# Optimization experiments

Measured on AMD Instinct MI355X. Metric: run time of the kernel, lower is better.

Reference implementation:

```python
import jax, jax.numpy as jnp
import numpy as np

N, C, H, W = 4, 256, 32, 32
NH = 2                      # att_nhead
HD = C // NH                # 128 per-head dim
MAX_DIS = 7
WS = 2 * MAX_DIS + 1        # 15 window side
WW = WS * WS                # 225 window positions
T = (C / NH) ** 0.5


def _gather_idx(h, w):
    # idx[wpos, m]: flat index into zero-padded (h+14, w+14) grid of the
    # neighbor at window offset wpos for query pixel m (== F.unfold semantics)
    pw = w + 2 * MAX_DIS
    dy, dx = np.meshgrid(np.arange(WS), np.arange(WS), indexing='ij')
    ys, xs = np.meshgrid(np.arange(h), np.arange(w), indexing='ij')
    idx = (dy.reshape(-1, 1) + ys.reshape(1, -1)) * pw + (dx.reshape(-1, 1) + xs.reshape(1, -1))
    return jnp.asarray(idx, dtype=jnp.int32)  # [WW, h*w]


def setup_inputs() -> dict:
    key = jax.random.key(0)
    ks = jax.random.split(key, 14)
    s = 0.02
    return {
        'q': jax.random.normal(ks[0], (N, C, H, W), jnp.float32),
        'k': jax.random.normal(ks[1], (N, C, H, W), jnp.float32),
        'v': jax.random.normal(ks[2], (N, C, H, W), jnp.float32),
        'Wq': jax.random.normal(ks[3], (C, C), jnp.float32) * s,
        'bq': jnp.zeros((C,), jnp.float32),
        'Wk': jax.random.normal(ks[4], (C, C), jnp.float32) * s,
        'bk': jnp.zeros((C,), jnp.float32),
        'Wv': jax.random.normal(ks[5], (C, C), jnp.float32) * s,
        'bv': jnp.zeros((C,), jnp.float32),
        'Wrel': jax.random.normal(ks[6], (NH, WW, HD), jnp.float32) * s,   # grouped 1x1 conv
        'brel': jnp.zeros((NH * WW,), jnp.float32),
        'V_bias': jax.random.normal(ks[7], (NH, HD, WW), jnp.float32) * s,
        'Wfc': jax.random.normal(ks[8], (C, C), jnp.float32) * s,
        'bfc': jnp.zeros((C,), jnp.float32),
    }


def _conv1x1(x, Wt, b):
    return jnp.einsum('nchw,dc->ndhw', x, Wt) + b[None, :, None, None]


def reference(q, k, v, Wq, bq, Wk, bk, Wv, bv, Wrel, brel, V_bias, Wfc, bfc):
    n, c, h, w = q.shape
    hw = h * w
    idx = _gather_idx(h, w)                                   # [WW, hw]
    pad = ((0, 0), (0, 0), (0, 0), (MAX_DIS, MAX_DIS), (MAX_DIS, MAX_DIS))

    q = _conv1x1(q, Wq, bq)
    k = _conv1x1(k, Wk, bk)
    v = _conv1x1(v, Wv, bv)

    # grouped 1x1 conv: relative position logits, [n, NH, WW, hw]
    rel = jnp.einsum('ngcxy,gwc->ngwxy', q.reshape(n, NH, HD, h, w), Wrel)
    rel = rel + brel.reshape(NH, WW)[None, :, :, None, None]
    rel = rel.reshape(n, NH, WW, hw)

    qs = (q / T).reshape(n, NH, HD, hw)

    # unfold K via zero-pad + gather: [n, NH, HD, WW, hw]
    k_pad = jnp.pad(k.reshape(n, NH, HD, h, w), pad).reshape(n, NH, HD, -1)
    k_un = k_pad[..., idx]
    qk = jnp.einsum('ngcm,ngcwm->ngwm', qs, k_un) + rel

    # boundary mask: neighbor inside the original image
    valid = jnp.pad(jnp.ones((h, w), jnp.float32), MAX_DIS).reshape(-1)[idx] > 0
    qk = jnp.where(valid[None, None], qk, jnp.float32(-1e8))
    attn = jax.nn.softmax(qk, axis=2)                         # over window positions

    agg_bias = jnp.einsum('ngwm,gcw->mngc', attn, V_bias).reshape(hw, n, c)

    # local2global scatter + dense einsum == gather of zero-padded V
    v_pad = jnp.pad(v.reshape(n, NH, HD, h, w), pad).reshape(n, NH, HD, -1)
    v_un = v_pad[..., idx]                                    # [n, NH, HD, WW, hw]
    agg_value = jnp.einsum('ngwm,ngcwm->mngc', attn, v_un).reshape(hw, n, c)

    out = (agg_value + agg_bias) @ Wfc.T + bfc                # [hw, n, c]
    return out
```

## Files before the change

### kernel.cpp

```cpp
#include <hip/hip_runtime.h>
#include <math.h>


typedef __attribute__((ext_vector_type(8))) short short8;
typedef __attribute__((ext_vector_type(4))) short short4v;
typedef __attribute__((ext_vector_type(4))) float floatx4;

__device__ __forceinline__ short f2bf(float f) {
    unsigned u = __float_as_uint(f);
    unsigned r = (u + 0x7fffu + ((u >> 16) & 1u)) >> 16;
    return (short)r;
}
__device__ __forceinline__ float bf2f(short s) {
    return __uint_as_float(((unsigned)(unsigned short)s) << 16);
}

__global__ __launch_bounds__(64)
void conv_w(const float* __restrict__ Wq, const float* __restrict__ Wk,
            const float* __restrict__ Wv, const float* __restrict__ Wfc,
            const float* __restrict__ Wrel, const float* __restrict__ Vb,
            short* __restrict__ Whi, short* __restrict__ Wlo,
            short* __restrict__ Wrh, short* __restrict__ Wrl,
            short* __restrict__ Vbh, short* __restrict__ Vbl)
{
    const int lane = threadIdx.x;
    const int n16 = lane & 15, quad = lane >> 4;
    const int z = blockIdx.z;

    if (z < 4) {
        const float* W = (z == 0 ? Wq : z == 1 ? Wk : z == 2 ? Wv : Wfc);
        const int dt = blockIdx.x, kc = blockIdx.y;
        const int d = dt * 16 + n16, cb = kc * 32 + quad * 8;
        float4 w0 = *(const float4*)&W[d * 256 + cb];
        float4 w1 = *(const float4*)&W[d * 256 + cb + 4];
        float f[8] = {w0.x, w0.y, w0.z, w0.w, w1.x, w1.y, w1.z, w1.w};
        short8 h8, l8;
#pragma unroll
        for (int j = 0; j < 8; ++j) {
            short hb = f2bf(f[j]);
            h8[j] = hb;
            l8[j] = f2bf(f[j] - bf2f(hb));
        }
        long off = (long)z * 65536 + (((long)(dt * 8 + kc) * 64) + lane) * 8;
        *(short8*)(Whi + off) = h8;
        *(short8*)(Wlo + off) = l8;
    } else if (z < 6) {
        const int g = z - 4;
        const int wt = blockIdx.x, kc = blockIdx.y;
        if (wt >= 15 || kc >= 4) return;
        const int w = wt * 16 + n16;
        const int cb = kc * 32 + quad * 8;
        float f[8] = {0.f, 0.f, 0.f, 0.f, 0.f, 0.f, 0.f, 0.f};
        if (w < 225) {
            float4 w0 = *(const float4*)&Wrel[(long)(g * 225 + w) * 128 + cb];
            float4 w1 = *(const float4*)&Wrel[(long)(g * 225 + w) * 128 + cb + 4];
            f[0] = w0.x; f[1] = w0.y; f[2] = w0.z; f[3] = w0.w;
            f[4] = w1.x; f[5] = w1.y; f[6] = w1.z; f[7] = w1.w;
        }
        short8 h8, l8;
#pragma unroll
        for (int j = 0; j < 8; ++j) {
            short hb = f2bf(f[j]);
            h8[j] = hb;
            l8[j] = f2bf(f[j] - bf2f(hb));
        }
        long off = (long)g * 30720 + (((long)(wt * 4 + kc) * 64) + lane) * 8;
        *(short8*)(Wrh + off) = h8;
        *(short8*)(Wrl + off) = l8;
    } else {
        const int g = z - 6;
        const int dt = blockIdx.x, wk = blockIdx.y;
        if (dt >= 8) return;
        const int ch = dt * 16 + n16;
        const int w0 = wk * 32 + quad * 8;
        float f[8];
#pragma unroll
        for (int j = 0; j < 8; ++j) {
            int w = w0 + j;
            f[j] = (w < 225) ? Vb[(long)(g * 128 + ch) * 225 + w] : 0.f;
        }
        short8 h8, l8;
#pragma unroll
        for (int j = 0; j < 8; ++j) {
            short hb = f2bf(f[j]);
            h8[j] = hb;
            l8[j] = f2bf(f[j] - bf2f(hb));
        }
        long off = (((long)(g * 128 + ch)) << 8) + w0;
        *(short8*)(Vbh + off) = h8;
        *(short8*)(Vbl + off) = l8;
    }
}

__global__ __launch_bounds__(256)
void mfma_proj(const float* __restrict__ q, const float* __restrict__ k,
               const float* __restrict__ v,
               const short* __restrict__ Whi, const short* __restrict__ Wlo,
               const float* __restrict__ bq, const float* __restrict__ bk,
               const float* __restrict__ bv,
               short* __restrict__ qhi, short* __restrict__ qlo,
               short* __restrict__ khi, short* __restrict__ klo,
               short* __restrict__ vhi, short* __restrict__ vlo)
{
    __shared__ float st[256 * 17];
    const int tid = threadIdx.x;
    const int wave = tid >> 6, lane = tid & 63;
    const int n16 = lane & 15, quad = lane >> 4;
    const int mt16 = blockIdx.x, z = blockIdx.y;
    const int sel = z >> 2, batch = z & 3;

    const float* X = (sel == 0 ? q : sel == 1 ? k : v) + ((long)batch << 18);

    {
        const float* src = X + ((long)tid << 10) + mt16 * 16;
        float4 a0 = *(const float4*)(src);
        float4 a1 = *(const float4*)(src + 4);
        float4 a2 = *(const float4*)(src + 8);
        float4 a3 = *(const float4*)(src + 12);
        float* d = &st[tid * 17];
        d[0] = a0.x; d[1] = a0.y; d[2] = a0.z; d[3] = a0.w;
        d[4] = a1.x; d[5] = a1.y; d[6] = a1.z; d[7] = a1.w;
        d[8] = a2.x; d[9] = a2.y; d[10] = a2.z; d[11] = a2.w;
        d[12] = a3.x; d[13] = a3.y; d[14] = a3.z; d[15] = a3.w;
    }

    const float* bias = (sel == 0 ? bq : sel == 1 ? bk : bv);
    float bbv[4][4];
#pragma unroll
    for (int i = 0; i < 4; ++i) {
        float4 b4 = *(const float4*)&bias[(wave * 4 + i) * 16 + quad * 4];
        bbv[i][0] = b4.x; bbv[i][1] = b4.y; bbv[i][2] = b4.z; bbv[i][3] = b4.w;
    }
    __syncthreads();

    floatx4 acc[4] = {{0.f,0.f,0.f,0.f},{0.f,0.f,0.f,0.f},
                      {0.f,0.f,0.f,0.f},{0.f,0.f,0.f,0.f}};
    const long abase = (long)sel * 65536 + (long)lane * 8;
#pragma unroll
    for (int kc = 0; kc < 8; ++kc) {
        short8 bh, bl;
        const float* col = &st[(kc * 32 + quad * 8) * 17 + n16];
#pragma unroll
        for (int j = 0; j < 8; ++j) {
            float f = col[j * 17];
            short hb = f2bf(f);
            bh[j] = hb;
            bl[j] = f2bf(f - bf2f(hb));
        }
#pragma unroll
        for (int i = 0; i < 4; ++i) {
            const int dt = wave * 4 + i;
            short8 ahi = *(const short8*)(Whi + abase + (long)(dt * 8 + kc) * 512);
            short8 alo = *(const short8*)(Wlo + abase + (long)(dt * 8 + kc) * 512);
            acc[i] = __builtin_amdgcn_mfma_f32_16x16x32_bf16(ahi, bh, acc[i], 0, 0, 0);
            acc[i] = __builtin_amdgcn_mfma_f32_16x16x32_bf16(ahi, bl, acc[i], 0, 0, 0);
            acc[i] = __builtin_amdgcn_mfma_f32_16x16x32_bf16(alo, bh, acc[i], 0, 0, 0);
        }
    }

    if (sel == 2) {
        const int m = mt16 * 16 + n16;
        const int yq = m >> 5, col = (m & 31) + 8;
#pragma unroll
        for (int i = 0; i < 4; ++i) {
            const int dt = wave * 4 + i;
#pragma unroll
            for (int r = 0; r < 4; ++r) {
                const int ch = dt * 16 + quad * 4 + r;
                const int gg = ch >> 7, chh = ch & 127;
                float f = acc[i][r] + bbv[i][r];
                short hb = f2bf(f);
                short lb = f2bf(f - bf2f(hb));
                long o = (((long)((batch * 2 + gg) * 128 + chh) * 32 + yq)) * 48 + col;
                vhi[o] = hb;
                vlo[o] = lb;
            }
        }
        {
            const int prow = mt16 >> 1, side = mt16 & 1;
            const int gg = tid >> 7, chp = tid & 127;
            long po = (((long)((batch * 2 + gg) * 128 + chp) * 32 + prow)) * 48 + side * 40;
            short8 zz = {0,0,0,0,0,0,0,0};
            *(short8*)(vhi + po) = zz;
            *(short8*)(vlo + po) = zz;
        }
        return;
    }

    __syncthreads();
    float* tile = st;
#pragma unroll
    for (int i = 0; i < 4; ++i) {
        const int dt = wave * 4 + i;
#pragma unroll
        for (int r = 0; r < 4; ++r)
            tile[n16 * 257 + dt * 16 + quad * 4 + r] = acc[i][r] + bbv[i][r];
    }
    __syncthreads();

    const float scale = (sel == 1) ? 0.08838834764831845f : 1.0f;
    const int m_l = tid >> 4, c16 = (tid & 15) * 16;
    const int m = mt16 * 16 + m_l;
    short* oh = sel ? khi : qhi;
    short* ol = sel ? klo : qlo;
#pragma unroll
    for (int half = 0; half < 2; ++half) {
        const int cg = c16 + half * 8;
        short8 h8, l8;
#pragma unroll
        for (int j = 0; j < 8; ++j) {
            float f = tile[m_l * 257 + cg + j] * scale;
            short hb = f2bf(f);
            h8[j] = hb;
            l8[j] = f2bf(f - bf2f(hb));
        }
        const int g = cg >> 7, ch = cg & 127;
        const long base = (((long)(batch * 2 + g) << 10) + m) * 128 + ch;
        *(short8*)(oh + base) = h8;
        *(short8*)(ol + base) = l8;
    }
}

__global__ __launch_bounds__(256)
void scores_pv(const short* __restrict__ qhi, const short* __restrict__ qlo,
               const short* __restrict__ khi, const short* __restrict__ klo,
               const short* __restrict__ Wrh, const short* __restrict__ Wrl,
               const float* __restrict__ brel,
               const short* __restrict__ vhi, const short* __restrict__ vlo,
               const short* __restrict__ Vbh, const short* __restrict__ Vbl,
               short* __restrict__ AGhi, short* __restrict__ AGlo)
{
    __shared__ __align__(16) float qk[16 * 241];
    __shared__ __align__(16) short pah[16 * 264];
    __shared__ __align__(16) short pal[16 * 264];
    __shared__ float invl[16];

    const int tid = threadIdx.x;
    const int wave = tid >> 6, lane = tid & 63;
    const int lin = blockIdx.x;
    const int bz  = lin & 7;
    const int yy  = lin >> 3;
    const int y   = yy >> 1;
    const int xt  = yy & 1;
    const int g = bz & 1;
    const int x0 = xt * 16;

    const int n16 = lane & 15, quad = lane >> 4;
    const long qbase = (((long)bz << 10) + y * 32 + x0 + n16) * 128 + quad * 8;
    short8 a_hi[4], a_lo[4];
#pragma unroll
    for (int ch = 0; ch < 4; ++ch) {
        a_hi[ch] = *(const short8*)(qhi + qbase + ch * 32);
        a_lo[ch] = *(const short8*)(qlo + qbase + ch * 32);
    }

    for (int wt = wave; wt < 15; wt += 4) {
        const short* Ah = Wrh + (long)g * 30720 + ((long)(wt * 4) * 64 + lane) * 8;
        const short* Al = Wrl + (long)g * 30720 + ((long)(wt * 4) * 64 + lane) * 8;
        floatx4 racc = {0.f, 0.f, 0.f, 0.f};
#pragma unroll
        for (int kc = 0; kc < 4; ++kc) {
            short8 whh = *(const short8*)(Ah + kc * 512);
            short8 wll = *(const short8*)(Al + kc * 512);
            racc = __builtin_amdgcn_mfma_f32_16x16x32_bf16(whh, a_hi[kc], racc, 0, 0, 0);
            racc = __builtin_amdgcn_mfma_f32_16x16x32_bf16(whh, a_lo[kc], racc, 0, 0, 0);
            racc = __builtin_amdgcn_mfma_f32_16x16x32_bf16(wll, a_hi[kc], racc, 0, 0, 0);
        }
#pragma unroll
        for (int r = 0; r < 4; ++r) {
            int w = wt * 16 + quad * 4 + r;
            if (w < 225) {
                int dy = w / 15, dx = w - dy * 15;
                qk[n16 * 241 + dy * 16 + dx] = racc[r] + brel[g * 225 + w];
            }
        }
    }
    __syncthreads();

    for (int e = tid; e < 16 * 241; e += 256) {
        int px = e / 241, idx = e - px * 241;
        int dy = idx >> 4, dx = idx & 15;
        int hy = y + dy - 7, hx = x0 + px + dx - 7;
        bool valid = (dx < 15) && (dy < 15) &&
                     (hy >= 0) && (hy < 32) && (hx >= 0) && (hx < 32);
        if (!valid) qk[e] = -1e8f;
    }
    __syncthreads();

    for (int dy = wave; dy < 15; dy += 4) {
        const int ky = y + dy - 7;
        if (ky < 0 || ky > 31) continue;
#pragma unroll
        for (int kxt = 0; kxt < 2; ++kxt) {
            const int kxg = x0 - 8 + kxt * 16 + n16;
            const long kb = (((long)bz << 10) + ky * 32 + kxg) * 128 + quad * 8;
            floatx4 acc = {0.f, 0.f, 0.f, 0.f};
#pragma unroll
            for (int ch = 0; ch < 4; ++ch) {
                short8 b_hi = *(const short8*)(khi + kb + ch * 32);
                short8 b_lo = *(const short8*)(klo + kb + ch * 32);
                acc = __builtin_amdgcn_mfma_f32_16x16x32_bf16(a_hi[ch], b_hi, acc, 0, 0, 0);
                acc = __builtin_amdgcn_mfma_f32_16x16x32_bf16(a_hi[ch], b_lo, acc, 0, 0, 0);
                acc = __builtin_amdgcn_mfma_f32_16x16x32_bf16(a_lo[ch], b_hi, acc, 0, 0, 0);
            }
            if (kxg >= 0 && kxg < 32) {
#pragma unroll
                for (int r = 0; r < 4; ++r) {
                    int m = quad * 4 + r;
                    int dx = kxg - (x0 + m) + 7;
                    if (dx >= 0 && dx < 15) {
                        int s = m * 241 + dy * 16 + dx;
                        qk[s] = qk[s] + acc[r];
                    }
                }
            }
        }
    }
    __syncthreads();

    {
        int px = tid >> 4, s = tid & 15;
        float mx = -3.0e38f;
        for (int w = s; w < 240; w += 16) mx = fmaxf(mx, qk[px * 241 + w]);
#pragma unroll
        for (int msk = 8; msk; msk >>= 1) mx = fmaxf(mx, __shfl_xor(mx, msk));
        float sum = 0.f;
        for (int w = s; w < 240; w += 16) {
            float p = __expf(qk[px * 241 + w] - mx);
            qk[px * 241 + w] = p;
            sum += p;
        }
#pragma unroll
        for (int msk = 8; msk; msk >>= 1) sum += __shfl_xor(sum, msk);
        if (s == 0) invl[px] = 1.0f / sum;
    }
    __syncthreads();

    for (int e = tid; e < 4096; e += 256) {
        int px = e >> 8, w = e & 255;
        float p = 0.f;
        if (w < 225) {
            int dy2 = w / 15, dx2 = w - dy2 * 15;
            p = qk[px * 241 + dy2 * 16 + dx2] * invl[px];
        }
        short hb = f2bf(p);
        pah[px * 264 + w] = hb;
        pal[px * 264 + w] = f2bf(p - bf2f(hb));
    }
    __syncthreads();

    floatx4 acc[2] = {{0.f,0.f,0.f,0.f},{0.f,0.f,0.f,0.f}};
    const int ch0a = (wave * 2) * 16;
    const int ch0b = (wave * 2 + 1) * 16;

#pragma unroll
    for (int wk = 0; wk < 8; ++wk) {
        short8 pa_h = *(const short8*)&pah[n16 * 264 + wk * 32 + quad * 8];
        short8 pa_l = *(const short8*)&pal[n16 * 264 + wk * 32 + quad * 8];
        const long vb0 = (((long)(g * 128 + ch0a + n16)) << 8) + wk * 32 + quad * 8;
        const long vb1 = (((long)(g * 128 + ch0b + n16)) << 8) + wk * 32 + quad * 8;
        short8 b0h = *(const short8*)(Vbh + vb0);
        short8 b0l = *(const short8*)(Vbl + vb0);
        short8 b1h = *(const short8*)(Vbh + vb1);
        short8 b1l = *(const short8*)(Vbl + vb1);
        acc[0] = __builtin_amdgcn_mfma_f32_16x16x32_bf16(pa_h, b0h, acc[0], 0, 0, 0);
        acc[0] = __builtin_amdgcn_mfma_f32_16x16x32_bf16(pa_h, b0l, acc[0], 0, 0, 0);
        acc[0] = __builtin_amdgcn_mfma_f32_16x16x32_bf16(pa_l, b0h, acc[0], 0, 0, 0);
        acc[1] = __builtin_amdgcn_mfma_f32_16x16x32_bf16(pa_h, b1h, acc[1], 0, 0, 0);
        acc[1] = __builtin_amdgcn_mfma_f32_16x16x32_bf16(pa_h, b1l, acc[1], 0, 0, 0);
        acc[1] = __builtin_amdgcn_mfma_f32_16x16x32_bf16(pa_l, b1h, acc[1], 0, 0, 0);
    }

    for (int dy = 0; dy < 15; ++dy) {
        const int ky = y + dy - 7;
        if (ky < 0 || ky > 31) continue;
        short8 bnd_h, bnd_l;
        const int rowoff = n16 * 264 + dy * 15 - n16 - 1;
#pragma unroll
        for (int j = 0; j < 8; ++j) {
            int kk = quad * 8 + j;
            int dx = kk - n16 - 1;
            bool valid = (unsigned)dx < 15u;
            int idx = valid ? (rowoff + kk) : 0;
            short vh = pah[idx];
            short vl = pal[idx];
            bnd_h[j] = valid ? vh : (short)0;
            bnd_l[j] = valid ? vl : (short)0;
        }
        const long v0o = (((long)((bz * 128 + ch0a + n16)) * 32 + ky)) * 48 + x0 + quad * 8;
        const long v1o = (((long)((bz * 128 + ch0b + n16)) * 32 + ky)) * 48 + x0 + quad * 8;
        short8 v0h = *(const short8*)(vhi + v0o);
        short8 v0l = *(const short8*)(vlo + v0o);
        short8 v1h = *(const short8*)(vhi + v1o);
        short8 v1l = *(const short8*)(vlo + v1o);
        acc[0] = __builtin_amdgcn_mfma_f32_16x16x32_bf16(bnd_h, v0h, acc[0], 0, 0, 0);
        acc[0] = __builtin_amdgcn_mfma_f32_16x16x32_bf16(bnd_h, v0l, acc[0], 0, 0, 0);
        acc[0] = __builtin_amdgcn_mfma_f32_16x16x32_bf16(bnd_l, v0h, acc[0], 0, 0, 0);
        acc[1] = __builtin_amdgcn_mfma_f32_16x16x32_bf16(bnd_h, v1h, acc[1], 0, 0, 0);
        acc[1] = __builtin_amdgcn_mfma_f32_16x16x32_bf16(bnd_h, v1l, acc[1], 0, 0, 0);
        acc[1] = __builtin_amdgcn_mfma_f32_16x16x32_bf16(bnd_l, v1h, acc[1], 0, 0, 0);
    }

    float* tile = qk;
#pragma unroll
    for (int t = 0; t < 2; ++t) {
        const int cb = (wave * 2 + t) * 16 + n16;
#pragma unroll
        for (int r = 0; r < 4; ++r)
            tile[(quad * 4 + r) * 133 + cb] = acc[t][r];
    }
    __syncthreads();

    const int sub = tid >> 6;
    short8 h8, l8;
#pragma unroll
    for (int j = 0; j < 8; ++j) {
        float f = tile[n16 * 133 + sub * 32 + quad * 8 + j];
        short hb = f2bf(f);
        h8[j] = hb;
        l8[j] = f2bf(f - bf2f(hb));
    }
    const int n = bz >> 1;
    const int mt16 = y * 2 + xt;
    const int kc = g * 4 + sub;
    long off = (long)n * 262144 + (((long)(mt16 * 8 + kc) * 64) + lane) * 8;
    *(short8*)(AGhi + off) = h8;
    *(short8*)(AGlo + off) = l8;
}

__global__ __launch_bounds__(256)
void mfma_fc(const short* __restrict__ Ahi, const short* __restrict__ Alo,
             const short* __restrict__ Whi, const short* __restrict__ Wlo,
             const float* __restrict__ bfc, float* __restrict__ out)
{
    __shared__ float tile[16 * 132];
    const int tid = threadIdx.x;
    const int wave = tid >> 6, lane = tid & 63;
    const int n16 = lane & 15, quad = lane >> 4;
    const int mt16 = blockIdx.x, db2 = blockIdx.y, nz = blockIdx.z;
    const int dt0 = db2 * 8 + wave * 2;

    const short* Bh = Ahi + (long)nz * 262144;
    const short* Bl = Alo + (long)nz * 262144;
    const long abase = (long)3 * 65536 + (long)lane * 8;

    float bbv[2][4];
#pragma unroll
    for (int p = 0; p < 2; ++p) {
        float4 b4 = *(const float4*)&bfc[(dt0 + p) * 16 + quad * 4];
        bbv[p][0] = b4.x; bbv[p][1] = b4.y; bbv[p][2] = b4.z; bbv[p][3] = b4.w;
    }

    floatx4 acc[2] = {{0.f,0.f,0.f,0.f},{0.f,0.f,0.f,0.f}};
#pragma unroll
    for (int kc = 0; kc < 8; ++kc) {
        const long bo = (long)(mt16 * 8 + kc) * 512 + (long)lane * 8;
        short8 bh = *(const short8*)(Bh + bo);
        short8 bl = *(const short8*)(Bl + bo);
#pragma unroll
        for (int p = 0; p < 2; ++p) {
            const int dt = dt0 + p;
            short8 ahi = *(const short8*)(Whi + abase + (long)(dt * 8 + kc) * 512);
            short8 alo = *(const short8*)(Wlo + abase + (long)(dt * 8 + kc) * 512);
            acc[p] = __builtin_amdgcn_mfma_f32_16x16x32_bf16(ahi, bh, acc[p], 0, 0, 0);
            acc[p] = __builtin_amdgcn_mfma_f32_16x16x32_bf16(ahi, bl, acc[p], 0, 0, 0);
            acc[p] = __builtin_amdgcn_mfma_f32_16x16x32_bf16(alo, bh, acc[p], 0, 0, 0);
        }
    }

#pragma unroll
    for (int p = 0; p < 2; ++p) {
        const int dl = (wave * 2 + p) * 16 + quad * 4;
#pragma unroll
        for (int r = 0; r < 4; ++r)
            tile[n16 * 132 + dl + r] = acc[p][r] + bbv[p][r];
    }
    __syncthreads();

    const int m_l = tid >> 4, d8 = (tid & 15) * 8;
    float4 o0 = *(const float4*)&tile[m_l * 132 + d8];
    float4 o1 = *(const float4*)&tile[m_l * 132 + d8 + 4];
    long ob = (long)(mt16 * 16 + m_l) * 1024 + nz * 256 + db2 * 128 + d8;
    *(float4*)&out[ob] = o0;
    *(float4*)&out[ob + 4] = o1;
}

extern "C" void kernel_launch(void* const* d_in, const int* in_sizes, int n_in,
                              void* d_out, int out_size, void* d_ws, size_t ws_size,
                              hipStream_t stream)
{
    const float* q    = (const float*)d_in[0];
    const float* k    = (const float*)d_in[1];
    const float* v    = (const float*)d_in[2];
    const float* Wq   = (const float*)d_in[3];
    const float* bq   = (const float*)d_in[4];
    const float* Wk   = (const float*)d_in[5];
    const float* bk   = (const float*)d_in[6];
    const float* Wv   = (const float*)d_in[7];
    const float* bv   = (const float*)d_in[8];
    const float* Wrel = (const float*)d_in[9];
    const float* brel = (const float*)d_in[10];
    const float* Vb   = (const float*)d_in[11];
    const float* Wfc  = (const float*)d_in[12];
    const float* bfc  = (const float*)d_in[13];
    float* out = (float*)d_out;

    float* ws   = (float*)d_ws;
    short* vhi  = (short*)(ws + 2097152);
    short* vlo  = (short*)(ws + 2883584);
    short* Vbh  = (short*)(ws + 4718592);
    short* Vbl  = (short*)(ws + 4751360);
    short* qhi  = (short*)(ws + 6561792);
    short* qlo  = (short*)(ws + 7086080);
    short* khi  = (short*)(ws + 7610368);
    short* klo  = (short*)(ws + 8134656);
    short* Whi  = (short*)(ws + 11804672);
    short* Wlo  = (short*)(ws + 11935744);
    short* AGhi = (short*)(ws + 12066816);
    short* AGlo = (short*)(ws + 12591104);
    short* Wrh  = (short*)(ws + 13115392);
    short* Wrl  = (short*)(ws + 13146112);

    conv_w<<<dim3(16, 8, 8), dim3(64), 0, stream>>>(Wq, Wk, Wv, Wfc, Wrel, Vb,
                                                    Whi, Wlo, Wrh, Wrl, Vbh, Vbl);

    mfma_proj<<<dim3(64, 12), dim3(256), 0, stream>>>(q, k, v, Whi, Wlo,
                                                      bq, bk, bv,
                                                      qhi, qlo, khi, klo,
                                                      vhi, vlo);

    scores_pv<<<dim3(512), dim3(256), 0, stream>>>(qhi, qlo, khi, klo,
                                                   Wrh, Wrl, brel,
                                                   vhi, vlo, Vbh, Vbl,
                                                   AGhi, AGlo);

    mfma_fc<<<dim3(64, 2, 4), dim3(256), 0, stream>>>(AGhi, AGlo, Whi, Wlo,
                                                      bfc, out);
}
```

Before: 162.4 us.

## Fold weight conversion into projection kernel and retile FC GEMM

Removes the separate conv_w launch. Projection blocks now read fp32 Wq/Wk/Wv directly and split them into bf16 hi/lo pairs in registers, while an extra grid row converts Wfc, Wrel and V_bias for the later kernels. The V output is staged through shared memory and written as vectorized short8 stores instead of scalar scatters. The FC kernel gives each wave one 16-wide output tile and launches twice as many blocks. This saves one launch and adds redundant in-register weight conversion across the 768 projection blocks.

```diff
diff --git a/kernel.cpp b/kernel.cpp
--- a/kernel.cpp
+++ b/kernel.cpp
@@ -15,101 +15,101 @@
     return __uint_as_float(((unsigned)(unsigned short)s) << 16);
 }
 
-__global__ __launch_bounds__(64)
-void conv_w(const float* __restrict__ Wq, const float* __restrict__ Wk,
-            const float* __restrict__ Wv, const float* __restrict__ Wfc,
-            const float* __restrict__ Wrel, const float* __restrict__ Vb,
-            short* __restrict__ Whi, short* __restrict__ Wlo,
-            short* __restrict__ Wrh, short* __restrict__ Wrl,
-            short* __restrict__ Vbh, short* __restrict__ Vbl)
-{
-    const int lane = threadIdx.x;
-    const int n16 = lane & 15, quad = lane >> 4;
-    const int z = blockIdx.z;
-
-    if (z < 4) {
-        const float* W = (z == 0 ? Wq : z == 1 ? Wk : z == 2 ? Wv : Wfc);
-        const int dt = blockIdx.x, kc = blockIdx.y;
-        const int d = dt * 16 + n16, cb = kc * 32 + quad * 8;
-        float4 w0 = *(const float4*)&W[d * 256 + cb];
-        float4 w1 = *(const float4*)&W[d * 256 + cb + 4];
-        float f[8] = {w0.x, w0.y, w0.z, w0.w, w1.x, w1.y, w1.z, w1.w};
-        short8 h8, l8;
-#pragma unroll
-        for (int j = 0; j < 8; ++j) {
-            short hb = f2bf(f[j]);
-            h8[j] = hb;
-            l8[j] = f2bf(f[j] - bf2f(hb));
-        }
-        long off = (long)z * 65536 + (((long)(dt * 8 + kc) * 64) + lane) * 8;
-        *(short8*)(Whi + off) = h8;
-        *(short8*)(Wlo + off) = l8;
-    } else if (z < 6) {
-        const int g = z - 4;
-        const int wt = blockIdx.x, kc = blockIdx.y;
-        if (wt >= 15 || kc >= 4) return;
-        const int w = wt * 16 + n16;
-        const int cb = kc * 32 + quad * 8;
-        float f[8] = {0.f, 0.f, 0.f, 0.f, 0.f, 0.f, 0.f, 0.f};
-        if (w < 225) {
-            float4 w0 = *(const float4*)&Wrel[(long)(g * 225 + w) * 128 + cb];
-            float4 w1 = *(const float4*)&Wrel[(long)(g * 225 + w) * 128 + cb + 4];
-            f[0] = w0.x; f[1] = w0.y; f[2] = w0.z; f[3] = w0.w;
-            f[4] = w1.x; f[5] = w1.y; f[6] = w1.z; f[7] = w1.w;
-        }
-        short8 h8, l8;
-#pragma unroll
-        for (int j = 0; j < 8; ++j) {
-            short hb = f2bf(f[j]);
-            h8[j] = hb;
-            l8[j] = f2bf(f[j] - bf2f(hb));
-        }
-        long off = (long)g * 30720 + (((long)(wt * 4 + kc) * 64) + lane) * 8;
-        *(short8*)(Wrh + off) = h8;
-        *(short8*)(Wrl + off) = l8;
-    } else {
-        const int g = z - 6;
-        const int dt = blockIdx.x, wk = blockIdx.y;
-        if (dt >= 8) return;
-        const int ch = dt * 16 + n16;
-        const int w0 = wk * 32 + quad * 8;
-        float f[8];
-#pragma unroll
-        for (int j = 0; j < 8; ++j) {
-            int w = w0 + j;
-            f[j] = (w < 225) ? Vb[(long)(g * 128 + ch) * 225 + w] : 0.f;
-        }
-        short8 h8, l8;
-#pragma unroll
-        for (int j = 0; j < 8; ++j) {
-            short hb = f2bf(f[j]);
-            h8[j] = hb;
-            l8[j] = f2bf(f[j] - bf2f(hb));
-        }
-        long off = (((long)(g * 128 + ch)) << 8) + w0;
-        *(short8*)(Vbh + off) = h8;
-        *(short8*)(Vbl + off) = l8;
-    }
-}
-
 __global__ __launch_bounds__(256)
 void mfma_proj(const float* __restrict__ q, const float* __restrict__ k,
                const float* __restrict__ v,
-               const short* __restrict__ Whi, const short* __restrict__ Wlo,
+               const float* __restrict__ Wq, const float* __restrict__ Wk,
+               const float* __restrict__ Wv, const float* __restrict__ Wfc,
+               const float* __restrict__ Wrel, const float* __restrict__ Vb,
                const float* __restrict__ bq, const float* __restrict__ bk,
                const float* __restrict__ bv,
                short* __restrict__ qhi, short* __restrict__ qlo,
                short* __restrict__ khi, short* __restrict__ klo,
-               short* __restrict__ vhi, short* __restrict__ vlo)
+               short* __restrict__ vhi, short* __restrict__ vlo,
+               short* __restrict__ Whi, short* __restrict__ Wlo,
+               short* __restrict__ Wrh, short* __restrict__ Wrl,
+               short* __restrict__ Vbh, short* __restrict__ Vbl)
 {
     __shared__ float st[256 * 17];
     const int tid = threadIdx.x;
     const int wave = tid >> 6, lane = tid & 63;
     const int n16 = lane & 15, quad = lane >> 4;
-    const int mt16 = blockIdx.x, z = blockIdx.y;
+    const int z = blockIdx.y;
+
+    if (z == 12) {
+#pragma unroll
+        for (int s = 0; s < 2; ++s) {
+            const int u = blockIdx.x * 8 + wave * 2 + s;
+            if (u < 128) {
+                const int dt = u >> 3, kc = u & 7;
+                const int d = dt * 16 + n16, cb = kc * 32 + quad * 8;
+                float4 w0 = *(const float4*)&Wfc[d * 256 + cb];
+                float4 w1 = *(const float4*)&Wfc[d * 256 + cb + 4];
+                float f[8] = {w0.x, w0.y, w0.z, w0.w, w1.x, w1.y, w1.z, w1.w};
+                short8 h8, l8;
+#pragma unroll
+                for (int j = 0; j < 8; ++j) {
+                    short hb = f2bf(f[j]);
+                    h8[j] = hb;
+                    l8[j] = f2bf(f[j] - bf2f(hb));
+                }
+                long off = (long)3 * 65536 + (((long)(dt * 8 + kc) * 64) + lane) * 8;
+                *(short8*)(Whi + off) = h8;
+                *(short8*)(Wlo + off) = l8;
+            } else if (u < 248) {
+                const int t = u - 128;
+                const int g = t / 60, r = t - g * 60;
+                const int wt = r >> 2, kc = r & 3;
+                const int w = wt * 16 + n16;
+                const int cb = kc * 32 + quad * 8;
+                float f[8] = {0.f, 0.f, 0.f, 0.f, 0.f, 0.f, 0.f, 0.f};
+                if (w < 225) {
+                    float4 w0 = *(const float4*)&Wrel[(long)(g * 225 + w) * 128 + cb];
+                    float4 w1 = *(const float4*)&Wrel[(long)(g * 225 + w) * 128 + cb + 4];
+                    f[0] = w0.x; f[1] = w0.y; f[2] = w0.z; f[3] = w0.w;
+                    f[4] = w1.x; f[5] = w1.y; f[6] = w1.z; f[7] = w1.w;
+                }
+                short8 h8, l8;
+#pragma unroll
+                for (int j = 0; j < 8; ++j) {
+                    short hb = f2bf(f[j]);
+                    h8[j] = hb;
+                    l8[j] = f2bf(f[j] - bf2f(hb));
+                }
+                long off = (long)g * 30720 + (((long)(wt * 4 + kc) * 64) + lane) * 8;
+                *(short8*)(Wrh + off) = h8;
+                *(short8*)(Wrl + off) = l8;
+            } else if (u < 376) {
+                const int t = u - 248;
+                const int g = t >> 6, r = t & 63;
+                const int dt = r >> 3, wk = r & 7;
+                const int ch = dt * 16 + n16;
+                const int w0 = wk * 32 + quad * 8;
+                float f[8];
+#pragma unroll
+                for (int j = 0; j < 8; ++j) {
+                    int w = w0 + j;
+                    f[j] = (w < 225) ? Vb[(long)(g * 128 + ch) * 225 + w] : 0.f;
+                }
+                short8 h8, l8;
+#pragma unroll
+                for (int j = 0; j < 8; ++j) {
+                    short hb = f2bf(f[j]);
+                    h8[j] = hb;
+                    l8[j] = f2bf(f[j] - bf2f(hb));
+                }
+                long off = (((long)(g * 128 + ch)) << 8) + w0;
+                *(short8*)(Vbh + off) = h8;
+                *(short8*)(Vbl + off) = l8;
+            }
+        }
+        return;
+    }
+
+    const int mt16 = blockIdx.x;
     const int sel = z >> 2, batch = z & 3;
-
     const float* X = (sel == 0 ? q : sel == 1 ? k : v) + ((long)batch << 18);
+    const float* Wsel = (sel == 0 ? Wq : sel == 1 ? Wk : Wv);
 
     {
         const float* src = X + ((long)tid << 10) + mt16 * 16;
@@ -135,7 +135,6 @@
 
     floatx4 acc[4] = {{0.f,0.f,0.f,0.f},{0.f,0.f,0.f,0.f},
                       {0.f,0.f,0.f,0.f},{0.f,0.f,0.f,0.f}};
-    const long abase = (long)sel * 65536 + (long)lane * 8;
 #pragma unroll
     for (int kc = 0; kc < 8; ++kc) {
         short8 bh, bl;
@@ -149,44 +148,24 @@
         }
 #pragma unroll
         for (int i = 0; i < 4; ++i) {
-            const int dt = wave * 4 + i;
-            short8 ahi = *(const short8*)(Whi + abase + (long)(dt * 8 + kc) * 512);
-            short8 alo = *(const short8*)(Wlo + abase + (long)(dt * 8 + kc) * 512);
+            const int d = (wave * 4 + i) * 16 + n16;
+            const float* wr = &Wsel[d * 256 + kc * 32 + quad * 8];
+            float4 w0 = *(const float4*)wr;
+            float4 w1 = *(const float4*)(wr + 4);
+            float f[8] = {w0.x, w0.y, w0.z, w0.w, w1.x, w1.y, w1.z, w1.w};
+            short8 ahi, alo;
+#pragma unroll
+            for (int j = 0; j < 8; ++j) {
+                short hb = f2bf(f[j]);
+                ahi[j] = hb;
+                alo[j] = f2bf(f[j] - bf2f(hb));
+            }
             acc[i] = __builtin_amdgcn_mfma_f32_16x16x32_bf16(ahi, bh, acc[i], 0, 0, 0);
             acc[i] = __builtin_amdgcn_mfma_f32_16x16x32_bf16(ahi, bl, acc[i], 0, 0, 0);
             acc[i] = __builtin_amdgcn_mfma_f32_16x16x32_bf16(alo, bh, acc[i], 0, 0, 0);
         }
     }
 
-    if (sel == 2) {
-        const int m = mt16 * 16 + n16;
-        const int yq = m >> 5, col = (m & 31) + 8;
-#pragma unroll
-        for (int i = 0; i < 4; ++i) {
-            const int dt = wave * 4 + i;
-#pragma unroll
-            for (int r = 0; r < 4; ++r) {
-                const int ch = dt * 16 + quad * 4 + r;
-                const int gg = ch >> 7, chh = ch & 127;
-                float f = acc[i][r] + bbv[i][r];
-                short hb = f2bf(f);
-                short lb = f2bf(f - bf2f(hb));
-                long o = (((long)((batch * 2 + gg) * 128 + chh) * 32 + yq)) * 48 + col;
-                vhi[o] = hb;
-                vlo[o] = lb;
-            }
-        }
-        {
-            const int prow = mt16 >> 1, side = mt16 & 1;
-            const int gg = tid >> 7, chp = tid & 127;
-            long po = (((long)((batch * 2 + gg) * 128 + chp) * 32 + prow)) * 48 + side * 40;
-            short8 zz = {0,0,0,0,0,0,0,0};
-            *(short8*)(vhi + po) = zz;
-            *(short8*)(vlo + po) = zz;
-        }
-        return;
-    }
-
     __syncthreads();
     float* tile = st;
 #pragma unroll
@@ -197,6 +176,31 @@
             tile[n16 * 257 + dt * 16 + quad * 4 + r] = acc[i][r] + bbv[i][r];
     }
     __syncthreads();
+
+    if (sel == 2) {
+        const int gg = tid >> 7, chp = tid & 127;
+        const int yq = mt16 >> 1, xb = (mt16 & 1) * 16;
+        short8 h0, h1, l0, l1;
+#pragma unroll
+        for (int j = 0; j < 8; ++j) {
+            float f0 = tile[j * 257 + tid];
+            float f1 = tile[(j + 8) * 257 + tid];
+            short hb0 = f2bf(f0), hb1 = f2bf(f1);
+            h0[j] = hb0; l0[j] = f2bf(f0 - bf2f(hb0));
+            h1[j] = hb1; l1[j] = f2bf(f1 - bf2f(hb1));
+        }
+        long o = ((long)((batch * 2 + gg) * 128 + chp) * 32 + yq) * 48 + 8 + xb;
+        *(short8*)(vhi + o) = h0;
+        *(short8*)(vhi + o + 8) = h1;
+        *(short8*)(vlo + o) = l0;
+        *(short8*)(vlo + o + 8) = l1;
+        const int prow = mt16 >> 1, side = mt16 & 1;
+        long po = ((long)((batch * 2 + gg) * 128 + chp) * 32 + prow) * 48 + side * 40;
+        short8 zz = {0,0,0,0,0,0,0,0};
+        *(short8*)(vhi + po) = zz;
+        *(short8*)(vlo + po) = zz;
+        return;
+    }
 
     const float scale = (sel == 1) ? 0.08838834764831845f : 1.0f;
     const int m_l = tid >> 4, c16 = (tid & 15) * 16;
@@ -433,56 +437,43 @@
              const short* __restrict__ Whi, const short* __restrict__ Wlo,
              const float* __restrict__ bfc, float* __restrict__ out)
 {
-    __shared__ float tile[16 * 132];
+    __shared__ float tile[16 * 68];
     const int tid = threadIdx.x;
     const int wave = tid >> 6, lane = tid & 63;
     const int n16 = lane & 15, quad = lane >> 4;
-    const int mt16 = blockIdx.x, db2 = blockIdx.y, nz = blockIdx.z;
-    const int dt0 = db2 * 8 + wave * 2;
-
+    const int mt16 = blockIdx.x, db = blockIdx.y, nz = blockIdx.z;
+    const int dt = db * 4 + wave;
+
+    const short* Ah = Whi + (long)3 * 65536 + ((long)(dt * 8) * 64 + lane) * 8;
+    const short* Al = Wlo + (long)3 * 65536 + ((long)(dt * 8) * 64 + lane) * 8;
     const short* Bh = Ahi + (long)nz * 262144;
     const short* Bl = Alo + (long)nz * 262144;
-    const long abase = (long)3 * 65536 + (long)lane * 8;
-
-    float bbv[2][4];
-#pragma unroll
-    for (int p = 0; p < 2; ++p) {
-        float4 b4 = *(const float4*)&bfc[(dt0 + p) * 16 + quad * 4];
-        bbv[p][0] = b4.x; bbv[p][1] = b4.y; bbv[p][2] = b4.z; bbv[p][3] = b4.w;
-    }
-
-    floatx4 acc[2] = {{0.f,0.f,0.f,0.f},{0.f,0.f,0.f,0.f}};
+
+    float4 bv4 = *(const float4*)&bfc[dt * 16 + quad * 4];
+    float bb[4] = {bv4.x, bv4.y, bv4.z, bv4.w};
+
+    floatx4 acc = {0.f, 0.f, 0.f, 0.f};
 #pragma unroll
     for (int kc = 0; kc < 8; ++kc) {
-        const long bo = (long)(mt16 * 8 + kc) * 512 + (long)lane * 8;
+        short8 ahi = *(const short8*)(Ah + kc * 512);
+        short8 alo = *(const short8*)(Al + kc * 512);
+        long bo = ((long)(mt16 * 8 + kc) * 64 + lane) * 8;
         short8 bh = *(const short8*)(Bh + bo);
         short8 bl = *(const short8*)(Bl + bo);
-#pragma unroll
-        for (int p = 0; p < 2; ++p) {
-            const int dt = dt0 + p;
-            short8 ahi = *(const short8*)(Whi + abase + (long)(dt * 8 + kc) * 512);
-            short8 alo = *(const short8*)(Wlo + abase + (long)(dt * 8 + kc) * 512);
-            acc[p] = __builtin_amdgcn_mfma_f32_16x16x32_bf16(ahi, bh, acc[p], 0, 0, 0);
-            acc[p] = __builtin_amdgcn_mfma_f32_16x16x32_bf16(ahi, bl, acc[p], 0, 0, 0);
-            acc[p] = __builtin_amdgcn_mfma_f32_16x16x32_bf16(alo, bh, acc[p], 0, 0, 0);
-        }
-    }
-
-#pragma unroll
-    for (int p = 0; p < 2; ++p) {
-        const int dl = (wave * 2 + p) * 16 + quad * 4;
-#pragma unroll
-        for (int r = 0; r < 4; ++r)
-            tile[n16 * 132 + dl + r] = acc[p][r] + bbv[p][r];
-    }
-    __syncthreads();
-
-    const int m_l = tid >> 4, d8 = (tid & 15) * 8;
-    float4 o0 = *(const float4*)&tile[m_l * 132 + d8];
-    float4 o1 = *(const float4*)&tile[m_l * 132 + d8 + 4];
-    long ob = (long)(mt16 * 16 + m_l) * 1024 + nz * 256 + db2 * 128 + d8;
-    *(float4*)&out[ob] = o0;
-    *(float4*)&out[ob + 4] = o1;
+        acc = __builtin_amdgcn_mfma_f32_16x16x32_bf16(ahi, bh, acc, 0, 0, 0);
+        acc = __builtin_amdgcn_mfma_f32_16x16x32_bf16(ahi, bl, acc, 0, 0, 0);
+        acc = __builtin_amdgcn_mfma_f32_16x16x32_bf16(alo, bh, acc, 0, 0, 0);
+    }
+
+    const int dl = wave * 16 + quad * 4;
+#pragma unroll
+    for (int r = 0; r < 4; ++r)
+        tile[n16 * 68 + dl + r] = acc[r] + bb[r];
+    __syncthreads();
+
+    const int mm = tid >> 4, d4 = (tid & 15) * 4;
+    float4 o4 = *(const float4*)&tile[mm * 68 + d4];
+    *(float4*)&out[(long)(mt16 * 16 + mm) * 1024 + nz * 256 + db * 64 + d4] = o4;
 }
 
 extern "C" void kernel_launch(void* const* d_in, const int* in_sizes, int n_in,
@@ -521,19 +512,19 @@
     short* Wrh  = (short*)(ws + 13115392);
     short* Wrl  = (short*)(ws + 13146112);
 
-    conv_w<<<dim3(16, 8, 8), dim3(64), 0, stream>>>(Wq, Wk, Wv, Wfc, Wrel, Vb,
-                                                    Whi, Wlo, Wrh, Wrl, Vbh, Vbl);
-
-    mfma_proj<<<dim3(64, 12), dim3(256), 0, stream>>>(q, k, v, Whi, Wlo,
+    mfma_proj<<<dim3(64, 13), dim3(256), 0, stream>>>(q, k, v,
+                                                      Wq, Wk, Wv, Wfc, Wrel, Vb,
                                                       bq, bk, bv,
                                                       qhi, qlo, khi, klo,
-                                                      vhi, vlo);
+                                                      vhi, vlo,
+                                                      Whi, Wlo, Wrh, Wrl,
+                                                      Vbh, Vbl);
 
     scores_pv<<<dim3(512), dim3(256), 0, stream>>>(qhi, qlo, khi, klo,
                                                    Wrh, Wrl, brel,
                                                    vhi, vlo, Vbh, Vbl,
                                                    AGhi, AGlo);
 
-    mfma_fc<<<dim3(64, 2, 4), dim3(256), 0, stream>>>(AGhi, AGlo, Whi, Wlo,
+    mfma_fc<<<dim3(64, 4, 4), dim3(256), 0, stream>>>(AGhi, AGlo, Whi, Wlo,
                                                       bfc, out);
 }
```

After: 168.7 us. 1.04x slower.
